# Optimization experiments

Hardware: AMD Instinct MI355X
Metric: run time of the kernel (lower is better)

The kernel has to match this reference:

```python
import jax, jax.numpy as jnp
import numpy as np

N_NODES = 100000
N_EDGES = 1600000
D_IN = 128
D_HID = 64
D_EMB = 64
EDGE_DIM = 2 * D_EMB  # 128
N_CASES = 4
BATCH = 16384
BN_EPS = 1e-5


def gcn_conv(x, src, dst, n, W, b):
    # PyG GCNConv: linear transform, add self-loops, sym-normalized aggregation
    h = x @ W  # [N, out]
    loop = jnp.arange(n, dtype=src.dtype)
    s = jnp.concatenate([src, loop])
    d = jnp.concatenate([dst, loop])
    deg = jax.ops.segment_sum(jnp.ones(s.shape[0], dtype=h.dtype), d, num_segments=n)
    dinv = jnp.where(deg > 0, deg ** -0.5, 0.0)
    norm = dinv[s] * dinv[d]  # [E+N]
    msg = h[s] * norm[:, None]
    return jax.ops.segment_sum(msg, d, num_segments=n) + b


def batchnorm(h, gamma, beta):
    # BatchNorm1d in training mode: biased batch statistics over nodes
    mu = h.mean(0)
    var = jnp.mean((h - mu) ** 2, axis=0)
    return (h - mu) * jax.lax.rsqrt(var + BN_EPS) * gamma + beta


def gcn_net(x, src, dst, n, W1, b1, g, be, W2, b2):
    h = gcn_conv(x, src, dst, n, W1, b1)
    h = jax.nn.relu(batchnorm(h, g, be))
    return gcn_conv(h, src, dst, n, W2, b2)


def setup_inputs() -> dict:
    key = jax.random.key(0)
    ks = jax.random.split(key, 20)
    inp = {
        "x": jax.random.normal(ks[0], (N_NODES, D_IN), dtype=jnp.float32),
        "edge_index": jax.random.randint(ks[1], (2, N_EDGES), 0, N_NODES, dtype=jnp.int32),
        "users_tensor": jax.random.randint(ks[2], (BATCH,), 0, 50000, dtype=jnp.int64) if jax.config.jax_enable_x64 else jax.random.randint(ks[2], (BATCH,), 0, 50000, dtype=jnp.int32),
        "items_tensor": jax.random.randint(ks[3], (BATCH,), 0, N_NODES, dtype=jnp.int32),
    }
    s = 0.05
    # generalized GCN params
    inp["W1g"] = jax.random.normal(ks[4], (D_IN, D_HID), dtype=jnp.float32) * s
    inp["b1g"] = jnp.zeros((D_HID,), jnp.float32)
    inp["g1g"] = jnp.ones((D_HID,), jnp.float32)
    inp["be1g"] = jnp.zeros((D_HID,), jnp.float32)
    inp["W2g"] = jax.random.normal(ks[5], (D_HID, D_EMB), dtype=jnp.float32) * s
    inp["b2g"] = jnp.zeros((D_EMB,), jnp.float32)
    # specific GCN params
    inp["W1s"] = jax.random.normal(ks[6], (D_IN, D_HID), dtype=jnp.float32) * s
    inp["b1s"] = jnp.zeros((D_HID,), jnp.float32)
    inp["g1s"] = jnp.ones((D_HID,), jnp.float32)
    inp["be1s"] = jnp.zeros((D_HID,), jnp.float32)
    inp["W2s"] = jax.random.normal(ks[7], (D_HID, D_EMB), dtype=jnp.float32) * s
    inp["b2s"] = jnp.zeros((D_EMB,), jnp.float32)
    # fusion gate (note: original forward uses hidden1 for BOTH inputs)
    inp["Wf1"] = jax.random.normal(ks[8], (EDGE_DIM, EDGE_DIM), dtype=jnp.float32) * s
    inp["Wsig"] = jax.random.normal(ks[9], (2 * EDGE_DIM, 1), dtype=jnp.float32) * s
    # heads
    inp["Wtc"] = jax.random.normal(ks[10], (EDGE_DIM, N_CASES), dtype=jnp.float32) * s
    inp["btc"] = jnp.zeros((N_CASES,), jnp.float32)
    inp["Wp"] = jax.random.normal(ks[11], (EDGE_DIM, 2), dtype=jnp.float32) * s
    inp["bp"] = jnp.zeros((2,), jnp.float32)
    return inp


def reference(x, edge_index, users_tensor, items_tensor,
              W1g, b1g, g1g, be1g, W2g, b2g,
              W1s, b1s, g1s, be1s, W2s, b2s,
              Wf1, Wsig, Wtc, btc, Wp, bp):
    n = x.shape[0]
    src, dst = edge_index[0], edge_index[1]

    nodes_gen = gcn_net(x, src, dst, n, W1g, b1g, g1g, be1g, W2g, b2g)  # [N, D_EMB]
    nodes_spec = gcn_net(x, src, dst, n, W1s, b1s, g1s, be1s, W2s, b2s)

    gen = jnp.concatenate([nodes_gen[users_tensor], nodes_gen[items_tensor]], axis=1)   # [B, 2E]
    spec = jnp.concatenate([nodes_spec[users_tensor], nodes_spec[items_tensor]], axis=1)

    h1 = jnp.tanh(gen @ Wf1)
    h2 = jnp.tanh(spec @ Wf1)  # original reuses hidden1
    z = jax.nn.sigmoid(jnp.concatenate([h1, h2], axis=1) @ Wsig)  # [B,1]
    fused = z * h1 + (1.0 - z) * h2

    link_output = fused @ Wp + bp
    generalized_output = gen @ Wtc + btc
    return (link_output, generalized_output)
```

## Files before the change

kernel.cpp:

```cpp
#include <hip/hip_runtime.h>
#include <hip/hip_bf16.h>


#define ELL_CAP 64
#define BCAP 8192
#define ACHUNK 5120

typedef __attribute__((ext_vector_type(8))) short short8v;
typedef __attribute__((ext_vector_type(4))) float f32x4;

static __device__ __forceinline__ unsigned short f2bf(float f) {
  unsigned u = __float_as_uint(f);
  unsigned r = (u + 0x7fffu + ((u >> 16) & 1u)) >> 16;
  return (unsigned short)r;
}
static __device__ __forceinline__ unsigned packbf(float a, float b) {
  return (unsigned)f2bf(a) | ((unsigned)f2bf(b) << 16);
}
static __device__ __forceinline__ float bflo(unsigned u) {
  return __uint_as_float(u << 16);
}
static __device__ __forceinline__ float bfhi(unsigned u) {
  return __uint_as_float(u & 0xffff0000u);
}
static __device__ __forceinline__ float bf2f(short s) {
  return __uint_as_float((unsigned)(unsigned short)s << 16);
}

__global__ void k_prep(const float* __restrict__ x, unsigned* __restrict__ bff,
                       int* __restrict__ gbump, float* __restrict__ stats,
                       const float* __restrict__ W1g, const float* __restrict__ b1g,
                       const float* __restrict__ W1s, const float* __restrict__ b1s,
                       const float* __restrict__ W2g, const float* __restrict__ b2g,
                       const float* __restrict__ W2s, const float* __restrict__ b2s,
                       const float* __restrict__ Wf1,
                       short* __restrict__ Wb1, short* __restrict__ Wb2,
                       short* __restrict__ WbH, float* __restrict__ bc1,
                       float* __restrict__ bc2, int n, int NB) {
  int idx = blockIdx.x * 256 + threadIdx.x;
  int n16 = n * 16;
  if (idx < n16) {
    const float4* f4 = (const float4*)x;
    float4 a = f4[idx * 2], b = f4[idx * 2 + 1];
    uint4 o;
    o.x = packbf(a.x, a.y);
    o.y = packbf(a.z, a.w);
    o.z = packbf(b.x, b.y);
    o.w = packbf(b.z, b.w);
    ((uint4*)bff)[idx] = o;
  }
  if (idx < 16384) {
    int k = idx >> 7, c = idx & 127;
    int pi = (k >> 3) * 1024 + c * 8 + (k & 7);
    float w1 = (c < 64) ? W1g[k * 64 + c] : W1s[k * 64 + (c - 64)];
    Wb1[pi] = (short)f2bf(w1);
    float w2 = 0.f;
    if (k < 64 && c < 64) w2 = W2g[k * 64 + c];
    else if (k >= 64 && c >= 64) w2 = W2s[(k - 64) * 64 + (c - 64)];
    Wb2[pi] = (short)f2bf(w2);
    WbH[pi] = (short)f2bf(Wf1[k * 128 + c]);
  }
  if (idx < 128) {
    bc1[idx] = (idx < 64) ? b1g[idx] : b1s[idx - 64];
    bc2[idx] = (idx < 64) ? b2g[idx] : b2s[idx - 64];
  }
  if (idx < NB) gbump[idx] = idx * BCAP;
  if (idx < 2048) stats[idx] = 0.f;
}

__global__ __launch_bounds__(256) void k_bucketA(
    const int* __restrict__ src, const int* __restrict__ dst,
    int* __restrict__ gbump, unsigned* __restrict__ ebuf, int E, int NB) {
  __shared__ int hist[512];
  __shared__ int gbase[512];
  int t = threadIdx.x;
  int e0 = blockIdx.x * ACHUNK;
  int m = min(ACHUNK, E - e0);
  for (int b = t; b < NB; b += 256) hist[b] = 0;
  __syncthreads();
  for (int i = t; i < m; i += 256) atomicAdd(&hist[dst[e0 + i] >> 8], 1);
  __syncthreads();
  for (int b = t; b < NB; b += 256) {
    gbase[b] = hist[b] ? atomicAdd(&gbump[b], hist[b]) : 0;
    hist[b] = 0;
  }
  __syncthreads();
  for (int i = t; i < m; i += 256) {
    int d = dst[e0 + i];
    int s = src[e0 + i];
    int b = d >> 8;
    int off = gbase[b] + atomicAdd(&hist[b], 1);
    if (off < (b + 1) * BCAP)
      ebuf[off] = ((unsigned)s << 8) | (unsigned)(d & 255);
  }
}

__global__ __launch_bounds__(256) void k_csrB(
    const unsigned* __restrict__ ebuf, const int* __restrict__ gbump,
    int* __restrict__ cnt, float* __restrict__ dinv, int* __restrict__ col,
    int n) {
  __shared__ int lbump[256];
  int b = blockIdx.x;
  lbump[threadIdx.x] = 0;
  __syncthreads();
  int base = b * BCAP;
  int m = min(gbump[b] - base, BCAP);
  for (int i = threadIdx.x; i < m; i += 256) {
    unsigned p = ebuf[base + i];
    int dloc = p & 255;
    int slot = atomicAdd(&lbump[dloc], 1);
    if (slot < ELL_CAP)
      col[(b * 256 + dloc) * ELL_CAP + slot] = (int)(p >> 8);
  }
  __syncthreads();
  int node = b * 256 + threadIdx.x;
  if (node < n) {
    int c = lbump[threadIdx.x];
    cnt[node] = min(c, ELL_CAP);
    dinv[node] = rsqrtf((float)(c + 1));
  }
}

template <bool BN>
__global__ __launch_bounds__(256) void k_agg(
    const unsigned* __restrict__ featb, unsigned* __restrict__ outb,
    const int* __restrict__ cnt, const float* __restrict__ dinv,
    const int* __restrict__ col,
    const float* __restrict__ stats, const float* __restrict__ g1g,
    const float* __restrict__ be1g, const float* __restrict__ g1s,
    const float* __restrict__ be1s, float inv_n, int n) {
  __shared__ float sc_sh[128], sf_sh[128];
  if (BN) {
    int c = threadIdx.x;
    if (c < 128) {
      float s = 0.f, q = 0.f;
#pragma unroll
      for (int k = 0; k < 8; k++) {
        s += stats[k * 256 + c];
        q += stats[k * 256 + 128 + c];
      }
      float mu = s * inv_n;
      float var = q * inv_n - mu * mu;
      float gam = (c < 64) ? g1g[c] : g1s[c - 64];
      float bet = (c < 64) ? be1g[c] : be1s[c - 64];
      float scv = gam * rsqrtf(var + 1e-5f);
      sc_sh[c] = scv;
      sf_sh[c] = bet - mu * scv;
    }
    __syncthreads();
  }
  int node = blockIdx.x * 16 + (threadIdx.x >> 4);
  if (node >= n) return;
  int t = threadIdx.x & 15;
  float sc[8], sf[8];
  if (BN) {
#pragma unroll
    for (int j = 0; j < 8; j++) {
      sc[j] = sc_sh[8 * t + j];
      sf[j] = sf_sh[8 * t + j];
    }
  }
  const uint4* f4 = (const uint4*)featb;
  float di = dinv[node];
  float acc[8];
  {
    uint4 sv = f4[node * 16 + t];
    float f[8] = {bflo(sv.x), bfhi(sv.x), bflo(sv.y), bfhi(sv.y),
                  bflo(sv.z), bfhi(sv.z), bflo(sv.w), bfhi(sv.w)};
#pragma unroll
    for (int j = 0; j < 8; j++) {
      if (BN) f[j] = fmaxf(f[j] * sc[j] + sf[j], 0.f);
      acc[j] = f[j] * di;
    }
  }
  int m = cnt[node];
  const int4* cl = (const int4*)&col[node * ELL_CAP];
  int i = 0;
  for (; i + 4 <= m; i += 4) {
    int4 c4 = cl[i >> 2];
    int ss[4] = {c4.x, c4.y, c4.z, c4.w};
#pragma unroll
    for (int q = 0; q < 4; q++) {
      int s = ss[q];
      float w = dinv[s];
      uint4 v = f4[s * 16 + t];
      float f[8] = {bflo(v.x), bfhi(v.x), bflo(v.y), bfhi(v.y),
                    bflo(v.z), bfhi(v.z), bflo(v.w), bfhi(v.w)};
#pragma unroll
      for (int j = 0; j < 8; j++) {
        if (BN) f[j] = fmaxf(f[j] * sc[j] + sf[j], 0.f);
        acc[j] += f[j] * w;
      }
    }
  }
  for (; i < m; ++i) {
    int s = col[node * ELL_CAP + i];
    float w = dinv[s];
    uint4 v = f4[s * 16 + t];
    float f[8] = {bflo(v.x), bfhi(v.x), bflo(v.y), bfhi(v.y),
                  bflo(v.z), bfhi(v.z), bflo(v.w), bfhi(v.w)};
#pragma unroll
    for (int j = 0; j < 8; j++) {
      if (BN) f[j] = fmaxf(f[j] * sc[j] + sf[j], 0.f);
      acc[j] += f[j] * w;
    }
  }
  uint4 o;
  o.x = packbf(acc[0] * di, acc[1] * di);
  o.y = packbf(acc[2] * di, acc[3] * di);
  o.z = packbf(acc[4] * di, acc[5] * di);
  o.w = packbf(acc[6] * di, acc[7] * di);
  ((uint4*)outb)[node * 16 + t] = o;
}

template <bool CBF16, bool STATS>
__global__ __launch_bounds__(256) void k_mgemm(
    const unsigned* __restrict__ Abf,
    const short* __restrict__ Wb, const float* __restrict__ bias,
    void* __restrict__ Cvp, int M, float* __restrict__ stats) {
  __shared__ short Wl[16384];
  __shared__ float shs[128], shq[128];
  {
    const uint4* s4 = (const uint4*)Wb;
    uint4* d4 = (uint4*)Wl;
    for (int i = threadIdx.x; i < 2048; i += 256) d4[i] = s4[i];
  }
  if (STATS && threadIdx.x < 128) { shs[threadIdx.x] = 0.f; shq[threadIdx.x] = 0.f; }
  __syncthreads();
  int lane = threadIdx.x & 63;
  int wv = threadIdx.x >> 6;
  int l15 = lane & 15;
  int l4 = lane >> 4;
  int row = blockIdx.x * 64 + wv * 16 + l15;
  int rc = min(row, M - 1);
  bool valid = row < M;

  short8v afr[4];
  const short* Ab = (const short*)Abf + (size_t)rc * 128;
#pragma unroll
  for (int ks = 0; ks < 4; ks++)
    afr[ks] = *(const short8v*)(Ab + ks * 32 + l4 * 8);

  f32x4 acc[8];
#pragma unroll
  for (int nt = 0; nt < 8; nt++) acc[nt] = (f32x4){0.f, 0.f, 0.f, 0.f};
#pragma unroll
  for (int nt = 0; nt < 8; nt++) {
#pragma unroll
    for (int ks = 0; ks < 4; ks++) {
      int kb = ks * 4 + l4;
      short8v w = *(const short8v*)&Wl[kb * 1024 + (nt * 16 + l15) * 8];
      acc[nt] = __builtin_amdgcn_mfma_f32_16x16x32_bf16(w, afr[ks], acc[nt], 0, 0, 0);
    }
  }

#pragma unroll
  for (int nt = 0; nt < 8; nt++) {
    int c0 = nt * 16 + l4 * 4;
    float o[4];
#pragma unroll
    for (int r = 0; r < 4; r++) o[r] = acc[nt][r];
    if (bias) {
      float4 bv = *(const float4*)(bias + c0);
      o[0] += bv.x; o[1] += bv.y; o[2] += bv.z; o[3] += bv.w;
    }
    if (STATS) {
      float s[4], q[4];
#pragma unroll
      for (int r = 0; r < 4; r++) {
        s[r] = valid ? o[r] : 0.f;
        q[r] = s[r] * s[r];
      }
#pragma unroll
      for (int m = 1; m < 16; m <<= 1) {
#pragma unroll
        for (int r = 0; r < 4; r++) {
          s[r] += __shfl_xor(s[r], m, 64);
          q[r] += __shfl_xor(q[r], m, 64);
        }
      }
      if (l15 == 0) {
#pragma unroll
        for (int r = 0; r < 4; r++) {
          atomicAdd(&shs[c0 + r], s[r]);
          atomicAdd(&shq[c0 + r], q[r]);
        }
      }
    }
    if (valid) {
      if (CBF16) {
        unsigned* Cb = (unsigned*)Cvp;
        uint2 p;
        p.x = packbf(o[0], o[1]);
        p.y = packbf(o[2], o[3]);
        *(uint2*)&Cb[(size_t)row * 64 + (c0 >> 1)] = p;
      } else {
        float* Cf = (float*)Cvp;
        *(float4*)&Cf[(size_t)row * 128 + c0] = make_float4(o[0], o[1], o[2], o[3]);
      }
    }
  }
  if (STATS) {
    __syncthreads();
    if (threadIdx.x < 128) {
      float* st = stats + (blockIdx.x & 7) * 256;
      atomicAdd(&st[threadIdx.x], shs[threadIdx.x]);
      atomicAdd(&st[128 + threadIdx.x], shq[threadIdx.x]);
    }
  }
}

__global__ __launch_bounds__(256) void k_fhead(
    const unsigned short* __restrict__ nodesb,
    const int* __restrict__ users, const int* __restrict__ items,
    const short* __restrict__ WbH, const float* __restrict__ Wsig,
    const float* __restrict__ Wtc, const float* __restrict__ btc,
    const float* __restrict__ Wp, const float* __restrict__ bp,
    float* __restrict__ out, int B) {
  __shared__ short Wl[16384];
  __shared__ float WsigL[256], WpL[256], WtcL[512];
  {
    const uint4* s4 = (const uint4*)WbH;
    uint4* d4 = (uint4*)Wl;
    for (int i = threadIdx.x; i < 2048; i += 256) d4[i] = s4[i];
    if (threadIdx.x < 256) {
      WsigL[threadIdx.x] = Wsig[threadIdx.x];
      WpL[threadIdx.x] = Wp[threadIdx.x];
    }
    for (int i = threadIdx.x; i < 512; i += 256) WtcL[i] = Wtc[i];
  }
  __syncthreads();
  int lane = threadIdx.x & 63;
  int wv = threadIdx.x >> 6;
  int l15 = lane & 15;
  int l4 = lane >> 4;
  int row = blockIdx.x * 64 + wv * 16 + l15;
  int rc = min(row, B - 1);
  int u = users[rc], it = items[rc];
  const short* pu = (const short*)nodesb + u * 128;
  const short* pi = (const short*)nodesb + it * 128;

  short8v ag[4], as[4];
#pragma unroll
  for (int ks = 0; ks < 4; ks++) {
    int k = ks * 32 + l4 * 8;
    const short* pg = (ks < 2) ? (pu + k) : (pi + (k - 64));
    const short* ps = (ks < 2) ? (pu + 64 + k) : (pi + k);
    ag[ks] = *(const short8v*)pg;
    as[ks] = *(const short8v*)ps;
  }

  f32x4 a1[8], a2[8];
#pragma unroll
  for (int nt = 0; nt < 8; nt++) {
    a1[nt] = (f32x4){0.f, 0.f, 0.f, 0.f};
    a2[nt] = (f32x4){0.f, 0.f, 0.f, 0.f};
  }
#pragma unroll
  for (int nt = 0; nt < 8; nt++) {
#pragma unroll
    for (int ks = 0; ks < 4; ks++) {
      int kb = ks * 4 + l4;
      short8v w = *(const short8v*)&Wl[kb * 1024 + (nt * 16 + l15) * 8];
      a1[nt] = __builtin_amdgcn_mfma_f32_16x16x32_bf16(w, ag[ks], a1[nt], 0, 0, 0);
      a2[nt] = __builtin_amdgcn_mfma_f32_16x16x32_bf16(w, as[ks], a2[nt], 0, 0, 0);
    }
  }

  float zp = 0.f;
#pragma unroll
  for (int nt = 0; nt < 8; nt++) {
    int c0 = nt * 16 + l4 * 4;
#pragma unroll
    for (int r = 0; r < 4; r++) {
      float h1 = tanhf(a1[nt][r]);
      float h2 = tanhf(a2[nt][r]);
      a1[nt][r] = h1;
      a2[nt][r] = h2;
      zp += h1 * WsigL[c0 + r] + h2 * WsigL[128 + c0 + r];
    }
  }
  zp += __shfl_xor(zp, 16, 64);
  zp += __shfl_xor(zp, 32, 64);
  float z = 1.f / (1.f + expf(-zp));

  float p0 = 0.f, p1 = 0.f;
#pragma unroll
  for (int nt = 0; nt < 8; nt++) {
    int c0 = nt * 16 + l4 * 4;
#pragma unroll
    for (int r = 0; r < 4; r++) {
      float fu = z * a1[nt][r] + (1.f - z) * a2[nt][r];
      p0 += fu * WpL[(c0 + r) * 2];
      p1 += fu * WpL[(c0 + r) * 2 + 1];
    }
  }
  float t0 = 0.f, t1 = 0.f, t2 = 0.f, t3 = 0.f;
#pragma unroll
  for (int ks = 0; ks < 4; ks++) {
    int kbase = ks * 32 + l4 * 8;
#pragma unroll
    for (int j = 0; j < 8; j++) {
      float g = bf2f(ag[ks][j]);
      int c = kbase + j;
      t0 += g * WtcL[c * 4];
      t1 += g * WtcL[c * 4 + 1];
      t2 += g * WtcL[c * 4 + 2];
      t3 += g * WtcL[c * 4 + 3];
    }
  }
  p0 += __shfl_xor(p0, 16, 64); p0 += __shfl_xor(p0, 32, 64);
  p1 += __shfl_xor(p1, 16, 64); p1 += __shfl_xor(p1, 32, 64);
  t0 += __shfl_xor(t0, 16, 64); t0 += __shfl_xor(t0, 32, 64);
  t1 += __shfl_xor(t1, 16, 64); t1 += __shfl_xor(t1, 32, 64);
  t2 += __shfl_xor(t2, 16, 64); t2 += __shfl_xor(t2, 32, 64);
  t3 += __shfl_xor(t3, 16, 64); t3 += __shfl_xor(t3, 32, 64);

  if (l4 == 0 && row < B) {
    out[row * 2] = p0 + bp[0];
    out[row * 2 + 1] = p1 + bp[1];
    float* go = out + 2 * B;
    go[row * 4] = t0 + btc[0];
    go[row * 4 + 1] = t1 + btc[1];
    go[row * 4 + 2] = t2 + btc[2];
    go[row * 4 + 3] = t3 + btc[3];
  }
}

extern "C" void kernel_launch(void* const* d_in, const int* in_sizes, int n_in,
                              void* d_out, int out_size, void* d_ws, size_t ws_size,
                              hipStream_t stream) {
  const float* x = (const float*)d_in[0];
  const int* ei = (const int*)d_in[1];
  const int* users = (const int*)d_in[2];
  const int* items = (const int*)d_in[3];
  const float* W1g = (const float*)d_in[4];
  const float* b1g = (const float*)d_in[5];
  const float* g1g = (const float*)d_in[6];
  const float* be1g = (const float*)d_in[7];
  const float* W2g = (const float*)d_in[8];
  const float* b2g = (const float*)d_in[9];
  const float* W1s = (const float*)d_in[10];
  const float* b1s = (const float*)d_in[11];
  const float* g1s = (const float*)d_in[12];
  const float* be1s = (const float*)d_in[13];
  const float* W2s = (const float*)d_in[14];
  const float* b2s = (const float*)d_in[15];
  const float* Wf1 = (const float*)d_in[16];
  const float* Wsig = (const float*)d_in[17];
  const float* Wtc = (const float*)d_in[18];
  const float* btc = (const float*)d_in[19];
  const float* Wp = (const float*)d_in[20];
  const float* bp = (const float*)d_in[21];

  int n = in_sizes[0] / 128;
  int E = in_sizes[1] / 2;
  int B = in_sizes[2];
  int NB = (n + 255) >> 8;
  const int* srcp = ei;
  const int* dstp = ei + E;
  float* out = (float*)d_out;

  char* w = (char*)d_ws;
  auto alloc = [&](size_t bytes) -> char* {
    char* p = w;
    w += (bytes + 255) & ~(size_t)255;
    return p;
  };
  unsigned* xab = (unsigned*)alloc((size_t)n * 64 * 4);
  float* big1 = (float*)alloc((size_t)n * 128 * 4);
  unsigned* bff = (unsigned*)alloc((size_t)n * 128 * 2);
  int* col = (int*)alloc((size_t)n * ELL_CAP * 4);
  unsigned* ebuf = (unsigned*)alloc((size_t)NB * BCAP * 4);
  int* cnt = (int*)alloc((size_t)n * 4);
  float* dinv = (float*)alloc((size_t)n * 4);
  int* gbump = (int*)alloc(512 * 4);
  short* Wb1 = (short*)alloc(16384 * 2);
  short* Wb2 = (short*)alloc(16384 * 2);
  short* WbH = (short*)alloc(16384 * 2);
  float* bc1 = (float*)alloc(512);
  float* bc2 = (float*)alloc(512);
  float* stats = (float*)alloc(2048 * 4);

  k_prep<<<(n * 16 + 255) / 256, 256, 0, stream>>>(
      x, bff, gbump, stats, W1g, b1g, W1s, b1s, W2g, b2g, W2s, b2s, Wf1,
      Wb1, Wb2, WbH, bc1, bc2, n, NB);
  k_bucketA<<<(E + ACHUNK - 1) / ACHUNK, 256, 0, stream>>>(srcp, dstp, gbump, ebuf, E, NB);
  k_csrB<<<NB, 256, 0, stream>>>(ebuf, gbump, cnt, dinv, col, n);

  unsigned* hb = (unsigned*)big1;
  unsigned short* nodesb = (unsigned short*)big1;

  k_agg<false><<<(n + 15) / 16, 256, 0, stream>>>(bff, xab, cnt, dinv, col,
                                                  nullptr, nullptr, nullptr,
                                                  nullptr, nullptr, 0.f, n);
  k_mgemm<true, true><<<(n + 63) / 64, 256, 0, stream>>>(xab, Wb1, bc1, hb, n, stats);

  k_agg<true><<<(n + 15) / 16, 256, 0, stream>>>(hb, xab, cnt, dinv, col,
                                                 stats, g1g, be1g, g1s, be1s,
                                                 1.f / (float)n, n);
  k_mgemm<true, false><<<(n + 63) / 64, 256, 0, stream>>>(xab, Wb2, bc2, nodesb, n, nullptr);

  k_fhead<<<(B + 63) / 64, 256, 0, stream>>>(nodesb, users, items, WbH, Wsig,
                                             Wtc, btc, Wp, bp, out, B);
}
```

Before: 250.5 us.

## Prescale features by dinv and pipeline neighbor gathers via async global-to-LDS loads

Moves the x-to-bf16 conversion after CSR build so each node's features can be prescaled by dinv, and adds a separate BN+ReLU+dinv fold pass before the second aggregation. The aggregation then only sums neighbor rows, with no per-edge dinv lookup or BN math. It issues the gathers as global_load_lds with a 4-deep software pipeline controlled by explicit waitcnt. The cost is two extra elementwise passes over node features and wave-uniform loop trip counts (max over 4 nodes per wave), with dummy loads of row 0 for padding slots.

```diff
diff --git a/kernel.cpp b/kernel.cpp
--- a/kernel.cpp
+++ b/kernel.cpp
@@ -27,8 +27,13 @@
   return __uint_as_float((unsigned)(unsigned short)s << 16);
 }
 
-__global__ void k_prep(const float* __restrict__ x, unsigned* __restrict__ bff,
-                       int* __restrict__ gbump, float* __restrict__ stats,
+static __device__ __forceinline__ void gload16(const unsigned* g, unsigned* l) {
+  __builtin_amdgcn_global_load_lds(
+      (const __attribute__((address_space(1))) unsigned*)g,
+      (__attribute__((address_space(3))) unsigned*)l, 16, 0, 0);
+}
+
+__global__ void k_prep(int* __restrict__ gbump, float* __restrict__ stats,
                        const float* __restrict__ W1g, const float* __restrict__ b1g,
                        const float* __restrict__ W1s, const float* __restrict__ b1s,
                        const float* __restrict__ W2g, const float* __restrict__ b2g,
@@ -36,19 +41,8 @@
                        const float* __restrict__ Wf1,
                        short* __restrict__ Wb1, short* __restrict__ Wb2,
                        short* __restrict__ WbH, float* __restrict__ bc1,
-                       float* __restrict__ bc2, int n, int NB) {
+                       float* __restrict__ bc2, int NB) {
   int idx = blockIdx.x * 256 + threadIdx.x;
-  int n16 = n * 16;
-  if (idx < n16) {
-    const float4* f4 = (const float4*)x;
-    float4 a = f4[idx * 2], b = f4[idx * 2 + 1];
-    uint4 o;
-    o.x = packbf(a.x, a.y);
-    o.y = packbf(a.z, a.w);
-    o.z = packbf(b.x, b.y);
-    o.w = packbf(b.z, b.w);
-    ((uint4*)bff)[idx] = o;
-  }
   if (idx < 16384) {
     int k = idx >> 7, c = idx & 127;
     int pi = (k >> 3) * 1024 + c * 8 + (k & 7);
@@ -121,16 +115,29 @@
   }
 }
 
-template <bool BN>
-__global__ __launch_bounds__(256) void k_agg(
-    const unsigned* __restrict__ featb, unsigned* __restrict__ outb,
-    const int* __restrict__ cnt, const float* __restrict__ dinv,
-    const int* __restrict__ col,
-    const float* __restrict__ stats, const float* __restrict__ g1g,
-    const float* __restrict__ be1g, const float* __restrict__ g1s,
-    const float* __restrict__ be1s, float inv_n, int n) {
+__global__ void k_xconv(const float* __restrict__ x, const float* __restrict__ dinv,
+                        unsigned* __restrict__ outp, int n16) {
+  int i = blockIdx.x * 256 + threadIdx.x;
+  if (i >= n16) return;
+  float dv = dinv[i >> 4];
+  const float4* f4 = (const float4*)x;
+  float4 a = f4[i * 2], b = f4[i * 2 + 1];
+  uint4 o;
+  o.x = packbf(a.x * dv, a.y * dv);
+  o.y = packbf(a.z * dv, a.w * dv);
+  o.z = packbf(b.x * dv, b.y * dv);
+  o.w = packbf(b.z * dv, b.w * dv);
+  ((uint4*)outp)[i] = o;
+}
+
+__global__ void k_bnfold(const unsigned* __restrict__ hb,
+                         const float* __restrict__ stats,
+                         const float* __restrict__ g1g, const float* __restrict__ be1g,
+                         const float* __restrict__ g1s, const float* __restrict__ be1s,
+                         const float* __restrict__ dinv,
+                         unsigned* __restrict__ outp, float inv_n, int n16) {
   __shared__ float sc_sh[128], sf_sh[128];
-  if (BN) {
+  {
     int c = threadIdx.x;
     if (c < 128) {
       float s = 0.f, q = 0.f;
@@ -149,68 +156,100 @@
     }
     __syncthreads();
   }
-  int node = blockIdx.x * 16 + (threadIdx.x >> 4);
-  if (node >= n) return;
-  int t = threadIdx.x & 15;
-  float sc[8], sf[8];
-  if (BN) {
-#pragma unroll
-    for (int j = 0; j < 8; j++) {
-      sc[j] = sc_sh[8 * t + j];
-      sf[j] = sf_sh[8 * t + j];
-    }
-  }
-  const uint4* f4 = (const uint4*)featb;
-  float di = dinv[node];
-  float acc[8];
+  int i = blockIdx.x * 256 + threadIdx.x;
+  if (i >= n16) return;
+  float dv = dinv[i >> 4];
+  int c8 = (i & 15) * 8;
+  uint4 v = ((const uint4*)hb)[i];
+  float f[8] = {bflo(v.x), bfhi(v.x), bflo(v.y), bfhi(v.y),
+                bflo(v.z), bfhi(v.z), bflo(v.w), bfhi(v.w)};
+  uint4 o;
+  float o0, o1;
+  o0 = fmaxf(f[0] * sc_sh[c8 + 0] + sf_sh[c8 + 0], 0.f) * dv;
+  o1 = fmaxf(f[1] * sc_sh[c8 + 1] + sf_sh[c8 + 1], 0.f) * dv;
+  o.x = packbf(o0, o1);
+  o0 = fmaxf(f[2] * sc_sh[c8 + 2] + sf_sh[c8 + 2], 0.f) * dv;
+  o1 = fmaxf(f[3] * sc_sh[c8 + 3] + sf_sh[c8 + 3], 0.f) * dv;
+  o.y = packbf(o0, o1);
+  o0 = fmaxf(f[4] * sc_sh[c8 + 4] + sf_sh[c8 + 4], 0.f) * dv;
+  o1 = fmaxf(f[5] * sc_sh[c8 + 5] + sf_sh[c8 + 5], 0.f) * dv;
+  o.z = packbf(o0, o1);
+  o0 = fmaxf(f[6] * sc_sh[c8 + 6] + sf_sh[c8 + 6], 0.f) * dv;
+  o1 = fmaxf(f[7] * sc_sh[c8 + 7] + sf_sh[c8 + 7], 0.f) * dv;
+  o.w = packbf(o0, o1);
+  ((uint4*)outp)[i] = o;
+}
+
+__global__ __launch_bounds__(128) void k_agg(
+    const unsigned* __restrict__ featp, unsigned* __restrict__ outb,
+    const int* __restrict__ cnt, const float* __restrict__ dinv,
+    const int* __restrict__ col, int n) {
+  __shared__ __align__(16) unsigned fbuf[2][4][256];
+  int lane = threadIdx.x & 63;
+  int wv = threadIdx.x >> 6;
+  int g = lane >> 4, t = lane & 15;
+  int node = blockIdx.x * 8 + wv * 4 + g;
+  int nodec = min(node, n - 1);
+  int cn = (node < n) ? cnt[nodec] : 0;
+  float di = dinv[nodec];
+  int m = cn + 1;
+  int mm = m;
+  mm = max(mm, __shfl_xor(mm, 16, 64));
+  mm = max(mm, __shfl_xor(mm, 32, 64));
+  int4 creg = ((const int4*)(col + (size_t)nodec * ELL_CAP))[t];
+  unsigned* myf = &fbuf[wv][0][0];
+  int gsel = g << 4;
+
+  gload16(featp + (size_t)nodec * 64 + t * 4, myf + 0 * 256);
   {
-    uint4 sv = f4[node * 16 + t];
-    float f[8] = {bflo(sv.x), bfhi(sv.x), bflo(sv.y), bfhi(sv.y),
-                  bflo(sv.z), bfhi(sv.z), bflo(sv.w), bfhi(sv.w)};
-#pragma unroll
-    for (int j = 0; j < 8; j++) {
-      if (BN) f[j] = fmaxf(f[j] * sc[j] + sf[j], 0.f);
-      acc[j] = f[j] * di;
-    }
-  }
-  int m = cnt[node];
-  const int4* cl = (const int4*)&col[node * ELL_CAP];
-  int i = 0;
-  for (; i + 4 <= m; i += 4) {
-    int4 c4 = cl[i >> 2];
-    int ss[4] = {c4.x, c4.y, c4.z, c4.w};
-#pragma unroll
-    for (int q = 0; q < 4; q++) {
-      int s = ss[q];
-      float w = dinv[s];
-      uint4 v = f4[s * 16 + t];
-      float f[8] = {bflo(v.x), bfhi(v.x), bflo(v.y), bfhi(v.y),
-                    bflo(v.z), bfhi(v.z), bflo(v.w), bfhi(v.w)};
-#pragma unroll
-      for (int j = 0; j < 8; j++) {
-        if (BN) f[j] = fmaxf(f[j] * sc[j] + sf[j], 0.f);
-        acc[j] += f[j] * w;
-      }
-    }
-  }
-  for (; i < m; ++i) {
-    int s = col[node * ELL_CAP + i];
-    float w = dinv[s];
-    uint4 v = f4[s * 16 + t];
-    float f[8] = {bflo(v.x), bfhi(v.x), bflo(v.y), bfhi(v.y),
-                  bflo(v.z), bfhi(v.z), bflo(v.w), bfhi(v.w)};
-#pragma unroll
-    for (int j = 0; j < 8; j++) {
-      if (BN) f[j] = fmaxf(f[j] * sc[j] + sf[j], 0.f);
-      acc[j] += f[j] * w;
-    }
-  }
-  uint4 o;
-  o.x = packbf(acc[0] * di, acc[1] * di);
-  o.y = packbf(acc[2] * di, acc[3] * di);
-  o.z = packbf(acc[4] * di, acc[5] * di);
-  o.w = packbf(acc[6] * di, acc[7] * di);
-  ((uint4*)outb)[node * 16 + t] = o;
+    int src = __shfl(creg.x, gsel, 64);
+    int idx = (1 <= cn && (unsigned)src < (unsigned)n) ? src : 0;
+    gload16(featp + (size_t)idx * 64 + t * 4, myf + 1 * 256);
+    src = __shfl(creg.y, gsel, 64);
+    idx = (2 <= cn && (unsigned)src < (unsigned)n) ? src : 0;
+    gload16(featp + (size_t)idx * 64 + t * 4, myf + 2 * 256);
+    src = __shfl(creg.z, gsel, 64);
+    idx = (3 <= cn && (unsigned)src < (unsigned)n) ? src : 0;
+    gload16(featp + (size_t)idx * 64 + t * 4, myf + 3 * 256);
+  }
+
+  float acc[8] = {0.f, 0.f, 0.f, 0.f, 0.f, 0.f, 0.f, 0.f};
+  for (int p0 = 0; p0 < mm; p0 += 4) {
+#pragma unroll
+    for (int u = 0; u < 4; u++) {
+      int p = p0 + u;
+      if (p >= mm) break;
+      asm volatile("s_waitcnt vmcnt(3)" ::: "memory");
+      __builtin_amdgcn_sched_barrier(0);
+      if (p < m) {
+        uint4 v = *(const uint4*)(myf + u * 256 + lane * 4);
+        acc[0] += bflo(v.x); acc[1] += bfhi(v.x);
+        acc[2] += bflo(v.y); acc[3] += bfhi(v.y);
+        acc[4] += bflo(v.z); acc[5] += bfhi(v.z);
+        acc[6] += bflo(v.w); acc[7] += bfhi(v.w);
+      }
+      asm volatile("s_waitcnt lgkmcnt(0)" ::: "memory");
+      __builtin_amdgcn_sched_barrier(0);
+      {
+        int b = p + 4;
+        int e = p + 3;
+        int j = (u + 3) & 3;
+        int cv = (j == 0) ? creg.x : (j == 1) ? creg.y : (j == 2) ? creg.z : creg.w;
+        int src = __shfl(cv, gsel + (e >> 2), 64);
+        int idx = (b <= cn && (unsigned)src < (unsigned)n) ? src : 0;
+        gload16(featp + (size_t)idx * 64 + t * 4, myf + u * 256);
+      }
+    }
+  }
+  asm volatile("s_waitcnt vmcnt(0)" ::: "memory");
+  if (node < n) {
+    uint4 o;
+    o.x = packbf(acc[0] * di, acc[1] * di);
+    o.y = packbf(acc[2] * di, acc[3] * di);
+    o.z = packbf(acc[4] * di, acc[5] * di);
+    o.w = packbf(acc[6] * di, acc[7] * di);
+    ((uint4*)outb)[(size_t)node * 16 + t] = o;
+  }
 }
 
 template <bool CBF16, bool STATS>
@@ -401,12 +440,12 @@
     int kbase = ks * 32 + l4 * 8;
 #pragma unroll
     for (int j = 0; j < 8; j++) {
-      float g = bf2f(ag[ks][j]);
+      float gv = bf2f(ag[ks][j]);
       int c = kbase + j;
-      t0 += g * WtcL[c * 4];
-      t1 += g * WtcL[c * 4 + 1];
-      t2 += g * WtcL[c * 4 + 2];
-      t3 += g * WtcL[c * 4 + 3];
+      t0 += gv * WtcL[c * 4];
+      t1 += gv * WtcL[c * 4 + 1];
+      t2 += gv * WtcL[c * 4 + 2];
+      t3 += gv * WtcL[c * 4 + 3];
     }
   }
   p0 += __shfl_xor(p0, 16, 64); p0 += __shfl_xor(p0, 32, 64);
@@ -482,23 +521,22 @@
   float* bc2 = (float*)alloc(512);
   float* stats = (float*)alloc(2048 * 4);
 
-  k_prep<<<(n * 16 + 255) / 256, 256, 0, stream>>>(
-      x, bff, gbump, stats, W1g, b1g, W1s, b1s, W2g, b2g, W2s, b2s, Wf1,
-      Wb1, Wb2, WbH, bc1, bc2, n, NB);
+  k_prep<<<64, 256, 0, stream>>>(gbump, stats, W1g, b1g, W1s, b1s, W2g, b2g,
+                                 W2s, b2s, Wf1, Wb1, Wb2, WbH, bc1, bc2, NB);
   k_bucketA<<<(E + ACHUNK - 1) / ACHUNK, 256, 0, stream>>>(srcp, dstp, gbump, ebuf, E, NB);
   k_csrB<<<NB, 256, 0, stream>>>(ebuf, gbump, cnt, dinv, col, n);
+  k_xconv<<<(n * 16 + 255) / 256, 256, 0, stream>>>(x, dinv, bff, n * 16);
 
   unsigned* hb = (unsigned*)big1;
   unsigned short* nodesb = (unsigned short*)big1;
 
-  k_agg<false><<<(n + 15) / 16, 256, 0, stream>>>(bff, xab, cnt, dinv, col,
-                                                  nullptr, nullptr, nullptr,
-                                                  nullptr, nullptr, 0.f, n);
+  k_agg<<<(n + 7) / 8, 128, 0, stream>>>(bff, xab, cnt, dinv, col, n);
   k_mgemm<true, true><<<(n + 63) / 64, 256, 0, stream>>>(xab, Wb1, bc1, hb, n, stats);
 
-  k_agg<true><<<(n + 15) / 16, 256, 0, stream>>>(hb, xab, cnt, dinv, col,
-                                                 stats, g1g, be1g, g1s, be1s,
-                                                 1.f / (float)n, n);
+  k_bnfold<<<(n * 16 + 255) / 256, 256, 0, stream>>>(hb, stats, g1g, be1g, g1s,
+                                                     be1s, dinv, bff,
+                                                     1.f / (float)n, n * 16);
+  k_agg<<<(n + 7) / 8, 128, 0, stream>>>(bff, xab, cnt, dinv, col, n);
   k_mgemm<true, false><<<(n + 63) / 64, 256, 0, stream>>>(xab, Wb2, bc2, nodesb, n, nullptr);
 
   k_fhead<<<(B + 63) / 64, 256, 0, stream>>>(nodesb, users, items, WbH, Wsig,
```

New measurement: 272.7 us. +8.9%, slower.

## Fuse sparse aggregation with following MFMA GEMM through LDS staging

Applied to the files above, without the earlier changes.

Merges the gather-aggregation kernel and the bf16 MFMA GEMM into one kernel per layer. Each block aggregates 64 node rows into a swizzled LDS tile and then runs the GEMM on it, which removes the intermediate global write and re-read plus two launches. Weights are now read directly from global/L1 rather than staged in LDS. The nt loop is no longer unrolled. Each thread now processes four nodes in sequence, which reduces gather parallelism per block and may lower latency hiding. Buffers are reassigned so that the second layer writes its output into the input bf16 buffer.

```diff
diff --git a/kernel.cpp b/kernel.cpp
--- a/kernel.cpp
+++ b/kernel.cpp
@@ -121,15 +121,19 @@
   }
 }
 
-template <bool BN>
-__global__ __launch_bounds__(256) void k_agg(
-    const unsigned* __restrict__ featb, unsigned* __restrict__ outb,
-    const int* __restrict__ cnt, const float* __restrict__ dinv,
-    const int* __restrict__ col,
-    const float* __restrict__ stats, const float* __restrict__ g1g,
-    const float* __restrict__ be1g, const float* __restrict__ g1s,
-    const float* __restrict__ be1s, float inv_n, int n) {
+template <bool STATS, bool CBF16, bool BN>
+__global__ __launch_bounds__(256) void k_aggemm(
+    const unsigned* __restrict__ featb, const int* __restrict__ cnt,
+    const float* __restrict__ dinv, const int* __restrict__ col,
+    const short* __restrict__ Wb, const float* __restrict__ bias,
+    void* __restrict__ Cvp, int n, float* __restrict__ stats,
+    const float* __restrict__ g1g, const float* __restrict__ be1g,
+    const float* __restrict__ g1s, const float* __restrict__ be1s,
+    float inv_n) {
+  __shared__ __align__(16) unsigned abuf[4096];
+  __shared__ float shs[128], shq[128];
   __shared__ float sc_sh[128], sf_sh[128];
+  if (STATS && threadIdx.x < 128) { shs[threadIdx.x] = 0.f; shq[threadIdx.x] = 0.f; }
   if (BN) {
     int c = threadIdx.x;
     if (c < 128) {
@@ -147,119 +151,107 @@
       sc_sh[c] = scv;
       sf_sh[c] = bet - mu * scv;
     }
-    __syncthreads();
-  }
-  int node = blockIdx.x * 16 + (threadIdx.x >> 4);
-  if (node >= n) return;
-  int t = threadIdx.x & 15;
-  float sc[8], sf[8];
-  if (BN) {
-#pragma unroll
-    for (int j = 0; j < 8; j++) {
-      sc[j] = sc_sh[8 * t + j];
-      sf[j] = sf_sh[8 * t + j];
-    }
-  }
-  const uint4* f4 = (const uint4*)featb;
-  float di = dinv[node];
-  float acc[8];
+  }
+  __syncthreads();
+
   {
-    uint4 sv = f4[node * 16 + t];
-    float f[8] = {bflo(sv.x), bfhi(sv.x), bflo(sv.y), bfhi(sv.y),
-                  bflo(sv.z), bfhi(sv.z), bflo(sv.w), bfhi(sv.w)};
-#pragma unroll
-    for (int j = 0; j < 8; j++) {
-      if (BN) f[j] = fmaxf(f[j] * sc[j] + sf[j], 0.f);
-      acc[j] = f[j] * di;
-    }
-  }
-  int m = cnt[node];
-  const int4* cl = (const int4*)&col[node * ELL_CAP];
-  int i = 0;
-  for (; i + 4 <= m; i += 4) {
-    int4 c4 = cl[i >> 2];
-    int ss[4] = {c4.x, c4.y, c4.z, c4.w};
-#pragma unroll
-    for (int q = 0; q < 4; q++) {
-      int s = ss[q];
-      float w = dinv[s];
-      uint4 v = f4[s * 16 + t];
-      float f[8] = {bflo(v.x), bfhi(v.x), bflo(v.y), bfhi(v.y),
-                    bflo(v.z), bfhi(v.z), bflo(v.w), bfhi(v.w)};
+    int t = threadIdx.x & 15;
+    int ng = threadIdx.x >> 4;
+    float sc[8], sf[8];
+    if (BN) {
 #pragma unroll
       for (int j = 0; j < 8; j++) {
-        if (BN) f[j] = fmaxf(f[j] * sc[j] + sf[j], 0.f);
-        acc[j] += f[j] * w;
-      }
-    }
-  }
-  for (; i < m; ++i) {
-    int s = col[node * ELL_CAP + i];
-    float w = dinv[s];
-    uint4 v = f4[s * 16 + t];
-    float f[8] = {bflo(v.x), bfhi(v.x), bflo(v.y), bfhi(v.y),
-                  bflo(v.z), bfhi(v.z), bflo(v.w), bfhi(v.w)};
-#pragma unroll
-    for (int j = 0; j < 8; j++) {
-      if (BN) f[j] = fmaxf(f[j] * sc[j] + sf[j], 0.f);
-      acc[j] += f[j] * w;
-    }
-  }
-  uint4 o;
-  o.x = packbf(acc[0] * di, acc[1] * di);
-  o.y = packbf(acc[2] * di, acc[3] * di);
-  o.z = packbf(acc[4] * di, acc[5] * di);
-  o.w = packbf(acc[6] * di, acc[7] * di);
-  ((uint4*)outb)[node * 16 + t] = o;
-}
-
-template <bool CBF16, bool STATS>
-__global__ __launch_bounds__(256) void k_mgemm(
-    const unsigned* __restrict__ Abf,
-    const short* __restrict__ Wb, const float* __restrict__ bias,
-    void* __restrict__ Cvp, int M, float* __restrict__ stats) {
-  __shared__ short Wl[16384];
-  __shared__ float shs[128], shq[128];
-  {
-    const uint4* s4 = (const uint4*)Wb;
-    uint4* d4 = (uint4*)Wl;
-    for (int i = threadIdx.x; i < 2048; i += 256) d4[i] = s4[i];
-  }
-  if (STATS && threadIdx.x < 128) { shs[threadIdx.x] = 0.f; shq[threadIdx.x] = 0.f; }
-  __syncthreads();
+        sc[j] = sc_sh[8 * t + j];
+        sf[j] = sf_sh[8 * t + j];
+      }
+    }
+    const uint4* f4 = (const uint4*)featb;
+    uint4* ab4 = (uint4*)abuf;
+    for (int sub = 0; sub < 4; sub++) {
+      int r = sub * 16 + ng;
+      int node = blockIdx.x * 64 + r;
+      int nodec = min(node, n - 1);
+      float di = dinv[nodec];
+      float acc[8];
+      {
+        uint4 sv = f4[nodec * 16 + t];
+        float f[8] = {bflo(sv.x), bfhi(sv.x), bflo(sv.y), bfhi(sv.y),
+                      bflo(sv.z), bfhi(sv.z), bflo(sv.w), bfhi(sv.w)};
+#pragma unroll
+        for (int j = 0; j < 8; j++) {
+          if (BN) f[j] = fmaxf(f[j] * sc[j] + sf[j], 0.f);
+          acc[j] = f[j] * di;
+        }
+      }
+      int m = cnt[nodec];
+      const int4* cl = (const int4*)&col[nodec * ELL_CAP];
+      int i = 0;
+      for (; i + 4 <= m; i += 4) {
+        int4 c4 = cl[i >> 2];
+        int ss[4] = {c4.x, c4.y, c4.z, c4.w};
+#pragma unroll
+        for (int q = 0; q < 4; q++) {
+          int s = ss[q];
+          float w = dinv[s];
+          uint4 v = f4[s * 16 + t];
+          float f[8] = {bflo(v.x), bfhi(v.x), bflo(v.y), bfhi(v.y),
+                        bflo(v.z), bfhi(v.z), bflo(v.w), bfhi(v.w)};
+#pragma unroll
+          for (int j = 0; j < 8; j++) {
+            if (BN) f[j] = fmaxf(f[j] * sc[j] + sf[j], 0.f);
+            acc[j] += f[j] * w;
+          }
+        }
+      }
+      for (; i < m; ++i) {
+        int s = col[nodec * ELL_CAP + i];
+        float w = dinv[s];
+        uint4 v = f4[s * 16 + t];
+        float f[8] = {bflo(v.x), bfhi(v.x), bflo(v.y), bfhi(v.y),
+                      bflo(v.z), bfhi(v.z), bflo(v.w), bfhi(v.w)};
+#pragma unroll
+        for (int j = 0; j < 8; j++) {
+          if (BN) f[j] = fmaxf(f[j] * sc[j] + sf[j], 0.f);
+          acc[j] += f[j] * w;
+        }
+      }
+      uint4 o;
+      o.x = packbf(acc[0] * di, acc[1] * di);
+      o.y = packbf(acc[2] * di, acc[3] * di);
+      o.z = packbf(acc[4] * di, acc[5] * di);
+      o.w = packbf(acc[6] * di, acc[7] * di);
+      ab4[r * 16 + (t ^ (r & 7))] = o;
+    }
+  }
+  __syncthreads();
+
   int lane = threadIdx.x & 63;
   int wv = threadIdx.x >> 6;
   int l15 = lane & 15;
   int l4 = lane >> 4;
-  int row = blockIdx.x * 64 + wv * 16 + l15;
-  int rc = min(row, M - 1);
-  bool valid = row < M;
+  int lrow = wv * 16 + l15;
+  int row = blockIdx.x * 64 + lrow;
+  bool valid = row < n;
+  const uint4* ab4 = (const uint4*)abuf;
 
   short8v afr[4];
-  const short* Ab = (const short*)Abf + (size_t)rc * 128;
 #pragma unroll
   for (int ks = 0; ks < 4; ks++)
-    afr[ks] = *(const short8v*)(Ab + ks * 32 + l4 * 8);
-
-  f32x4 acc[8];
-#pragma unroll
-  for (int nt = 0; nt < 8; nt++) acc[nt] = (f32x4){0.f, 0.f, 0.f, 0.f};
-#pragma unroll
+    afr[ks] = *(const short8v*)&ab4[lrow * 16 + ((ks * 4 + l4) ^ (lrow & 7))];
+
+#pragma unroll 1
   for (int nt = 0; nt < 8; nt++) {
+    f32x4 a = (f32x4){0.f, 0.f, 0.f, 0.f};
 #pragma unroll
     for (int ks = 0; ks < 4; ks++) {
       int kb = ks * 4 + l4;
-      short8v w = *(const short8v*)&Wl[kb * 1024 + (nt * 16 + l15) * 8];
-      acc[nt] = __builtin_amdgcn_mfma_f32_16x16x32_bf16(w, afr[ks], acc[nt], 0, 0, 0);
-    }
-  }
-
-#pragma unroll
-  for (int nt = 0; nt < 8; nt++) {
+      short8v w = *(const short8v*)&Wb[kb * 1024 + (nt * 16 + l15) * 8];
+      a = __builtin_amdgcn_mfma_f32_16x16x32_bf16(w, afr[ks], a, 0, 0, 0);
+    }
     int c0 = nt * 16 + l4 * 4;
     float o[4];
 #pragma unroll
-    for (int r = 0; r < 4; r++) o[r] = acc[nt][r];
+    for (int r = 0; r < 4; r++) o[r] = a[r];
     if (bias) {
       float4 bv = *(const float4*)(bias + c0);
       o[0] += bv.x; o[1] += bv.y; o[2] += bv.z; o[3] += bv.w;
@@ -401,12 +393,12 @@
     int kbase = ks * 32 + l4 * 8;
 #pragma unroll
     for (int j = 0; j < 8; j++) {
-      float g = bf2f(ag[ks][j]);
+      float gv = bf2f(ag[ks][j]);
       int c = kbase + j;
-      t0 += g * WtcL[c * 4];
-      t1 += g * WtcL[c * 4 + 1];
-      t2 += g * WtcL[c * 4 + 2];
-      t3 += g * WtcL[c * 4 + 3];
+      t0 += gv * WtcL[c * 4];
+      t1 += gv * WtcL[c * 4 + 1];
+      t2 += gv * WtcL[c * 4 + 2];
+      t3 += gv * WtcL[c * 4 + 3];
     }
   }
   p0 += __shfl_xor(p0, 16, 64); p0 += __shfl_xor(p0, 32, 64);
@@ -467,9 +459,8 @@
     w += (bytes + 255) & ~(size_t)255;
     return p;
   };
-  unsigned* xab = (unsigned*)alloc((size_t)n * 64 * 4);
+  unsigned* bff = (unsigned*)alloc((size_t)n * 128 * 2);
   float* big1 = (float*)alloc((size_t)n * 128 * 4);
-  unsigned* bff = (unsigned*)alloc((size_t)n * 128 * 2);
   int* col = (int*)alloc((size_t)n * ELL_CAP * 4);
   unsigned* ebuf = (unsigned*)alloc((size_t)NB * BCAP * 4);
   int* cnt = (int*)alloc((size_t)n * 4);
@@ -489,17 +480,15 @@
   k_csrB<<<NB, 256, 0, stream>>>(ebuf, gbump, cnt, dinv, col, n);
 
   unsigned* hb = (unsigned*)big1;
-  unsigned short* nodesb = (unsigned short*)big1;
-
-  k_agg<false><<<(n + 15) / 16, 256, 0, stream>>>(bff, xab, cnt, dinv, col,
-                                                  nullptr, nullptr, nullptr,
-                                                  nullptr, nullptr, 0.f, n);
-  k_mgemm<true, true><<<(n + 63) / 64, 256, 0, stream>>>(xab, Wb1, bc1, hb, n, stats);
-
-  k_agg<true><<<(n + 15) / 16, 256, 0, stream>>>(hb, xab, cnt, dinv, col,
-                                                 stats, g1g, be1g, g1s, be1s,
-                                                 1.f / (float)n, n);
-  k_mgemm<true, false><<<(n + 63) / 64, 256, 0, stream>>>(xab, Wb2, bc2, nodesb, n, nullptr);
+  unsigned short* nodesb = (unsigned short*)bff;
+
+  k_aggemm<true, true, false><<<(n + 63) / 64, 256, 0, stream>>>(
+      bff, cnt, dinv, col, Wb1, bc1, hb, n, stats,
+      nullptr, nullptr, nullptr, nullptr, 0.f);
+
+  k_aggemm<false, true, true><<<(n + 63) / 64, 256, 0, stream>>>(
+      hb, cnt, dinv, col, Wb2, bc2, nodesb, n, stats,
+      g1g, be1g, g1s, be1s, 1.f / (float)n);
 
   k_fhead<<<(B + 63) / 64, 256, 0, stream>>>(nodesb, users, items, WbH, Wsig,
                                              Wtc, btc, Wp, bp, out, B);
```

Measured after the change: 242.2 us. 1.03x faster.
